# Kernel optimization log

Measured on AMD Instinct MI355X. Metric: run time of the kernel, lower is better.

## Reference

```python
import jax, jax.numpy as jnp
import numpy as np

B, N, E, D, AD = 2, 4096, 4, 64, 32


def setup_inputs() -> dict:
    key = jax.random.key(0)
    ks = jax.random.split(key, 10)
    s = 0.02  # init std matching module _initialization
    return {
        "prop_state": jax.random.normal(ks[0], (B, N, D), jnp.float32),
        "annotation": jax.random.normal(ks[1], (B, N, AD), jnp.float32),
        "A": jax.random.uniform(ks[2], (B, N, N * E), jnp.float32),
        "W_in": jax.random.normal(ks[3], (E, D, D), jnp.float32) * s,
        "b_in": jnp.zeros((E, D), jnp.float32),
        "Wr": jax.random.normal(ks[4], (D, 2 * D), jnp.float32) * s,
        "br": jnp.zeros((D,), jnp.float32),
        "Wz": jax.random.normal(ks[5], (D, 2 * D), jnp.float32) * s,
        "bz": jnp.zeros((D,), jnp.float32),
        "Wh": jax.random.normal(ks[6], (D, 2 * D), jnp.float32) * s,
        "bh": jnp.zeros((D,), jnp.float32),
        "Wo1": jax.random.normal(ks[7], (D, D + AD), jnp.float32) * s,
        "bo1": jnp.zeros((D,), jnp.float32),
        "Wo2": jax.random.normal(ks[8], (1, D), jnp.float32) * s,
        "bo2": jnp.zeros((1,), jnp.float32),
    }


def reference(prop_state, annotation, A, W_in, b_in, Wr, br, Wz, bz, Wh, bh, Wo1, bo1, Wo2, bo2):
    b, n, d = prop_state.shape
    e = W_in.shape[0]
    # per-edge-type input transforms: [B, E, N, D] -> [B, E*N, D] (edge-type major)
    in_states = jnp.einsum('bnd,eod->beno', prop_state, W_in) + b_in[None, :, None, :]
    in_flat = in_states.reshape(b, e * n, d)
    # dense adjacency aggregation: A [B, N, N*E] x in_flat [B, N*E, D]
    a_in = jnp.einsum('bnm,bmd->bnd', A, in_flat)
    # GRU-style gated node update
    a = jnp.concatenate([a_in, prop_state], axis=-1)  # [B, N, 2D]
    r = jax.nn.sigmoid(a @ Wr.T + br)
    z = jax.nn.sigmoid(a @ Wz.T + bz)
    h_hat = jnp.tanh(jnp.concatenate([a_in, r * prop_state], axis=-1) @ Wh.T + bh)
    new_state = (1.0 - z) * prop_state + z * h_hat  # [B, N, D]
    # output head
    join = jnp.concatenate([new_state, annotation], axis=-1)  # [B, N, D+AD]
    h = jnp.tanh(join @ Wo1.T + bo1)
    out = (h @ Wo2.T + bo2).sum(axis=2)  # [B, N]
    return out
```

## Files before the change

kernel.cpp:

```cpp
#include <hip/hip_runtime.h>
#include <hip/hip_bf16.h>
#include <stdint.h>

typedef __bf16 bf16x8 __attribute__((ext_vector_type(8)));
typedef float  f32x16 __attribute__((ext_vector_type(16)));
typedef float  f32x4  __attribute__((ext_vector_type(4)));

static constexpr int Bz = 2, Nn = 4096, Ee = 4, Dd = 64, ADim = 32;
static constexpr int Mm = Nn * Ee;
static constexpr int KSEG = 8;
static constexpr int KLEN = Mm / KSEG;
static constexpr int NT = Bz * Nn / 32;
static constexpr size_t SEGSTRIDE = (size_t)NT * 32 * 64;
static constexpr int PHK = 256;
static constexpr int NPH = KLEN / PHK;

__device__ __forceinline__ bf16x8 cvt8(float4 a, float4 b) {
  bf16x8 r;
  r[0] = (__bf16)a.x; r[1] = (__bf16)a.y; r[2] = (__bf16)a.z; r[3] = (__bf16)a.w;
  r[4] = (__bf16)b.x; r[5] = (__bf16)b.y; r[6] = (__bf16)b.z; r[7] = (__bf16)b.w;
  return r;
}
__device__ __forceinline__ bf16x8 cvt8v(f32x4 a, f32x4 b) {
  bf16x8 r;
  r[0] = (__bf16)a[0]; r[1] = (__bf16)a[1]; r[2] = (__bf16)a[2]; r[3] = (__bf16)a[3];
  r[4] = (__bf16)b[0]; r[5] = (__bf16)b[1]; r[6] = (__bf16)b[2]; r[7] = (__bf16)b[3];
  return r;
}
__device__ __forceinline__ f32x16 zero16() {
  f32x16 z;
#pragma unroll
  for (int i = 0; i < 16; ++i) z[i] = 0.f;
  return z;
}
__device__ __forceinline__ f32x16 mm(bf16x8 a, bf16x8 b, f32x16 c) {
  return __builtin_amdgcn_mfma_f32_32x32x16_bf16(a, b, c, 0, 0, 0);
}
__device__ __forceinline__ float sigm(float x) { return 1.f / (1.f + __expf(-x)); }
__device__ __forceinline__ float tanh_fast(float x) {
  float e = __expf(2.f * x);
  return 1.f - 2.f / (e + 1.f);
}
__device__ __forceinline__ void async_lds16(const void* g, void* l) {
  __builtin_amdgcn_global_load_lds(
      (const __attribute__((address_space(1))) uint32_t*)g,
      (__attribute__((address_space(3))) uint32_t*)l, 16, 0, 0);
}

__global__ __launch_bounds__(256) void k_packbt(
    const float* __restrict__ prop, const float* __restrict__ Win,
    const float* __restrict__ bin, __bf16* __restrict__ Bt,
    const float* __restrict__ Wr, const float* __restrict__ Wz,
    const float* __restrict__ Wh, const float* __restrict__ Wo1,
    __bf16* __restrict__ Wp) {
  const int bid = blockIdx.x;
  const int tid = threadIdx.x;
  const int w = tid >> 6, l = tid & 63;
  const int r31 = l & 31, h = l >> 5;

  if (bid == 512) {
    for (int f = w; f < 60; f += 4) {
      const float* W; int L, fl;
      if (f < 16)      { W = Wr;  L = 128; fl = f; }
      else if (f < 32) { W = Wz;  L = 128; fl = f - 16; }
      else if (f < 48) { W = Wh;  L = 128; fl = f - 32; }
      else             { W = Wo1; L = 96;  fl = f - 48; }
      const int ks = fl >> 1, oh = fl & 1;
      const float* src = W + (size_t)(32 * oh + r31) * L + 16 * ks + 8 * h;
      float4 s0 = *reinterpret_cast<const float4*>(src);
      float4 s1 = *reinterpret_cast<const float4*>(src + 4);
      *reinterpret_cast<bf16x8*>(Wp + ((size_t)f * 64 + l) * 8) = cvt8(s0, s1);
    }
    return;
  }
  const int nchunk = bid & 63;
  const int e = (bid >> 6) & 3, b = bid >> 8;
  const int oh = w & 1, ns = w >> 1;
  const int o_row = oh * 32 + r31;
  const int n_col = nchunk * 64 + ns * 32 + r31;
  const float* wbase = Win + ((size_t)e * 64 + o_row) * 64 + 8 * h;
  const float* pbase = prop + ((size_t)b * Nn + n_col) * 64 + 8 * h;
  f32x16 acc = zero16();
#pragma unroll
  for (int ks = 0; ks < 4; ++ks) {
    float4 w0 = *reinterpret_cast<const float4*>(wbase + 16 * ks);
    float4 w1 = *reinterpret_cast<const float4*>(wbase + 16 * ks + 4);
    float4 p0 = *reinterpret_cast<const float4*>(pbase + 16 * ks);
    float4 p1 = *reinterpret_cast<const float4*>(pbase + 16 * ks + 4);
    acc = mm(cvt8(w0, w1), cvt8(p0, p1), acc);
  }
#pragma unroll
  for (int reg = 0; reg < 16; ++reg) {
    int orow = oh * 32 + (reg & 3) + 8 * (reg >> 2) + 4 * h;
    float v = acc[reg] + bin[e * 64 + orow];
    Bt[((size_t)b * 64 + orow) * Mm + (size_t)e * Nn + n_col] = (__bf16)v;
  }
}

__global__ __launch_bounds__(512, 1) void k_big_gemm(
    const float* __restrict__ A, const __bf16* __restrict__ Bt,
    __bf16* __restrict__ part) {
  __shared__ float  ahalf[2][64][PHK];
  __shared__ __bf16 btl[64][PHK];

  const int bid = blockIdx.x;
  const int kseg = bid & 7;
  const int tg   = bid >> 3;
  const int bb   = tg >> 4;
  const int gg   = tg & 15;
  const int ph0  = tg & (NPH - 1);
  const int tid = threadIdx.x;
  const int w = tid >> 6, l = tid & 63;
  const int r31 = l & 31, h = l >> 5;
  const int tp = w >> 2, q = (w >> 1) & 1, kh = w & 1;

  const size_t kbase = (size_t)kseg * KLEN;
  const float*  Ab  = A  + ((size_t)bb * Nn + gg * 256) * Mm + kbase;
  const __bf16* BtB = Bt + (size_t)bb * 64 * Mm + kbase;

#define ISSUE_A(pi, pr, hf)                                                  \
  { _Pragma("unroll")                                                        \
    for (int j_ = 0; j_ < 8; ++j_) {                                         \
      const int rw_ = 8 * w + j_;                                            \
      const float* src_ = Ab + (size_t)((pi) * 64 + rw_) * Mm +              \
                          (size_t)(pr) * PHK + ((l ^ (rw_ & 7)) << 2);       \
      async_lds16(src_, (void*)&ahalf[hf][rw_][0]);                          \
    } }

  bf16x8 btreg[4];
  const int btrh = l >> 5;
  const int btu  = l & 31;
#define LOAD_BT(pr)                                                          \
  { _Pragma("unroll")                                                        \
    for (int j_ = 0; j_ < 4; ++j_) {                                         \
      const int row_ = 8 * w + 2 * j_ + btrh;                                \
      btreg[j_] = *reinterpret_cast<const bf16x8*>(                          \
          BtB + (size_t)row_ * Mm + (size_t)(pr) * PHK + btu * 8);           \
    } }
#define WRITE_BT                                                             \
  { _Pragma("unroll")                                                        \
    for (int j_ = 0; j_ < 4; ++j_) {                                         \
      const int row_ = 8 * w + 2 * j_ + btrh;                                \
      *reinterpret_cast<bf16x8*>(&btl[row_][(btu ^ (row_ & 7)) * 8]) =       \
          btreg[j_];                                                         \
    } }

  const int swz  = r31 & 7;
  const int arow = tp * 32 + r31;
  const int brow = 32 * q + r31;
  f32x16 acc[4] = {zero16(), zero16(), zero16(), zero16()};

#define COMPUTE(pi, hf)                                                      \
  { _Pragma("unroll")                                                        \
    for (int s_ = 0; s_ < 8; ++s_) {                                         \
      const int ua_ = kh * 32 + 4 * s_ + 2 * h;                              \
      f32x4 fa0 = *reinterpret_cast<const f32x4*>(                           \
          &ahalf[hf][arow][((ua_ ^ swz) << 2)]);                             \
      f32x4 fa1 = *reinterpret_cast<const f32x4*>(                           \
          &ahalf[hf][arow][(((ua_ + 1) ^ swz) << 2)]);                       \
      const int ub_ = kh * 16 + 2 * s_ + h;                                  \
      bf16x8 fb = *reinterpret_cast<const bf16x8*>(                          \
          &btl[brow][((ub_ ^ swz) * 8)]);                                    \
      acc[pi] = mm(cvt8v(fa0, fa1), fb, acc[pi]);                            \
    } }

  LOAD_BT(ph0);
  ISSUE_A(0, ph0, 0);
  ISSUE_A(1, ph0, 1);
  asm volatile("s_waitcnt vmcnt(16)" ::: "memory");
  WRITE_BT;
  asm volatile("s_waitcnt vmcnt(8) lgkmcnt(0)" ::: "memory");
  __builtin_amdgcn_s_barrier();

  for (int pp = 0; pp < NPH; ++pp) {
    const bool lastp = (pp == NPH - 1);
    const int prc = (pp + ph0) & (NPH - 1);
    const int prn = (pp + 1 + ph0) & (NPH - 1);
    COMPUTE(0, 0);
    __builtin_amdgcn_s_barrier();
    ISSUE_A(2, prc, 0);
    asm volatile("s_waitcnt vmcnt(8)" ::: "memory");
    __builtin_amdgcn_s_barrier();
    COMPUTE(1, 1);
    __builtin_amdgcn_s_barrier();
    if (!lastp) LOAD_BT(prn);
    ISSUE_A(3, prc, 1);
    asm volatile("s_waitcnt vmcnt(8)" ::: "memory");
    __builtin_amdgcn_s_barrier();
    COMPUTE(2, 0);
    __builtin_amdgcn_s_barrier();
    if (!lastp) {
      ISSUE_A(0, prn, 0);
      asm volatile("s_waitcnt vmcnt(8)" ::: "memory");
    } else {
      asm volatile("s_waitcnt vmcnt(0)" ::: "memory");
    }
    __builtin_amdgcn_s_barrier();
    COMPUTE(3, 1);
    if (!lastp) {
      __builtin_amdgcn_s_barrier();
      WRITE_BT;
      ISSUE_A(1, prn, 1);
      asm volatile("s_waitcnt vmcnt(8) lgkmcnt(0)" ::: "memory");
      __builtin_amdgcn_s_barrier();
    }
  }
#undef ISSUE_A
#undef LOAD_BT
#undef WRITE_BT
#undef COMPUTE

  float* scratch = &ahalf[0][0][0];
  if (kh == 1) {
#pragma unroll
    for (int i = 0; i < 4; ++i) {
      float* slot = scratch + (size_t)(i * 4 + tp * 2 + q) * 1024 + l * 16;
#pragma unroll
      for (int r = 0; r < 16; r += 4) {
        f32x4 v; v[0] = acc[i][r]; v[1] = acc[i][r + 1];
        v[2] = acc[i][r + 2]; v[3] = acc[i][r + 3];
        *reinterpret_cast<f32x4*>(slot + r) = v;
      }
    }
  }
  __syncthreads();
  if (kh == 0) {
#pragma unroll
    for (int i = 0; i < 4; ++i) {
      const int tile = bb * 128 + gg * 8 + i * 2 + tp;
      __bf16* pb = part + (size_t)kseg * SEGSTRIDE + (size_t)tile * 32 * 64 + 32 * q;
      const float* slot = scratch + (size_t)(i * 4 + tp * 2 + q) * 1024 + l * 16;
#pragma unroll
      for (int reg = 0; reg < 16; ++reg) {
        int row = (reg & 3) + 8 * (reg >> 2) + 4 * h;
        pb[row * 64 + r31] = (__bf16)(acc[i][reg] + slot[reg]);
      }
    }
  }
}

__global__ __launch_bounds__(64) void k_gru(
    const __bf16* __restrict__ part, const float* __restrict__ prop,
    const float* __restrict__ annot, const __bf16* __restrict__ Wp,
    const float* __restrict__ br, const float* __restrict__ bz,
    const float* __restrict__ bh, const float* __restrict__ bo1,
    const float* __restrict__ Wo2, const float* __restrict__ bo2,
    float* __restrict__ out) {
  __shared__ float plds[32][68];
  __shared__ float tlds[32][68];
  const int tile = blockIdx.x;
  const int R0 = tile * 32;
  const int l = threadIdx.x;
  const int r31 = l & 31, h = l >> 5;

  bf16x8 xa[4], xp[4], xan[2];
  {
    const __bf16* pt = part + ((size_t)tile * 32 + r31) * 64 + 8 * h;
    const float* pb = prop + (size_t)(R0 + r31) * 64 + 8 * h;
#pragma unroll
    for (int ks = 0; ks < 4; ++ks) {
      float s[8] = {0.f, 0.f, 0.f, 0.f, 0.f, 0.f, 0.f, 0.f};
#pragma unroll
      for (int seg = 0; seg < KSEG; ++seg) {
        bf16x8 v = *reinterpret_cast<const bf16x8*>(pt + seg * SEGSTRIDE + 16 * ks);
#pragma unroll
        for (int j = 0; j < 8; ++j) s[j] += (float)v[j];
      }
      bf16x8 x;
#pragma unroll
      for (int j = 0; j < 8; ++j) x[j] = (__bf16)s[j];
      xa[ks] = x;
      float4 p0 = *reinterpret_cast<const float4*>(pb + 16 * ks);
      float4 p1 = *reinterpret_cast<const float4*>(pb + 16 * ks + 4);
      xp[ks] = cvt8(p0, p1);
      *reinterpret_cast<float4*>(&plds[r31][16 * ks + 8 * h]) = p0;
      *reinterpret_cast<float4*>(&plds[r31][16 * ks + 8 * h + 4]) = p1;
    }
    const float* anb = annot + (size_t)(R0 + r31) * ADim + 8 * h;
#pragma unroll
    for (int ks = 0; ks < 2; ++ks) {
      float4 a0 = *reinterpret_cast<const float4*>(anb + 16 * ks);
      float4 a1 = *reinterpret_cast<const float4*>(anb + 16 * ks + 4);
      xan[ks] = cvt8(a0, a1);
    }
  }
  __syncthreads();

#define LDWP(base, ks, oh) \
  (*reinterpret_cast<const bf16x8*>(Wp + (((size_t)(base) + (ks) * 2 + (oh)) * 64 + l) * 8))

  f32x16 aR[2] = {zero16(), zero16()}, aZ[2] = {zero16(), zero16()};
#pragma unroll
  for (int ks = 0; ks < 8; ++ks) {
    bf16x8 af = (ks < 4) ? xa[ks] : xp[ks - 4];
#pragma unroll
    for (int oh = 0; oh < 2; ++oh) {
      aR[oh] = mm(af, LDWP(0, ks, oh), aR[oh]);
      aZ[oh] = mm(af, LDWP(16, ks, oh), aZ[oh]);
    }
  }
  const float br_[2] = {br[r31], br[32 + r31]};
  const float bz_[2] = {bz[r31], bz[32 + r31]};
  float propv[2][16], zv[2][16];
#pragma unroll
  for (int oh = 0; oh < 2; ++oh) {
#pragma unroll
    for (int reg = 0; reg < 16; ++reg) {
      int row = (reg & 3) + 8 * (reg >> 2) + 4 * h;
      int o = 32 * oh + r31;
      propv[oh][reg] = plds[row][o];
      float rv = sigm(aR[oh][reg] + br_[oh]);
      zv[oh][reg] = sigm(aZ[oh][reg] + bz_[oh]);
      tlds[row][o] = rv * propv[oh][reg];
    }
  }
  __syncthreads();
  bf16x8 xr[4];
#pragma unroll
  for (int ks = 0; ks < 4; ++ks) {
    float4 t0 = *reinterpret_cast<const float4*>(&tlds[r31][16 * ks + 8 * h]);
    float4 t1 = *reinterpret_cast<const float4*>(&tlds[r31][16 * ks + 8 * h + 4]);
    xr[ks] = cvt8(t0, t1);
  }
  f32x16 aH[2] = {zero16(), zero16()};
#pragma unroll
  for (int ks = 0; ks < 8; ++ks) {
    bf16x8 af = (ks < 4) ? xa[ks] : xr[ks - 4];
#pragma unroll
    for (int oh = 0; oh < 2; ++oh) aH[oh] = mm(af, LDWP(32, ks, oh), aH[oh]);
  }
  __syncthreads();
  const float bh_[2] = {bh[r31], bh[32 + r31]};
#pragma unroll
  for (int oh = 0; oh < 2; ++oh) {
#pragma unroll
    for (int reg = 0; reg < 16; ++reg) {
      int row = (reg & 3) + 8 * (reg >> 2) + 4 * h;
      int o = 32 * oh + r31;
      float hh = tanh_fast(aH[oh][reg] + bh_[oh]);
      float z = zv[oh][reg];
      tlds[row][o] = (1.f - z) * propv[oh][reg] + z * hh;
    }
  }
  __syncthreads();
  bf16x8 xn[4];
#pragma unroll
  for (int ks = 0; ks < 4; ++ks) {
    float4 t0 = *reinterpret_cast<const float4*>(&tlds[r31][16 * ks + 8 * h]);
    float4 t1 = *reinterpret_cast<const float4*>(&tlds[r31][16 * ks + 8 * h + 4]);
    xn[ks] = cvt8(t0, t1);
  }
  f32x16 aO[2] = {zero16(), zero16()};
#pragma unroll
  for (int ks = 0; ks < 6; ++ks) {
    bf16x8 af = (ks < 4) ? xn[ks] : xan[ks - 4];
#pragma unroll
    for (int oh = 0; oh < 2; ++oh) aO[oh] = mm(af, LDWP(48, ks, oh), aO[oh]);
  }
  const float bo1_[2] = {bo1[r31], bo1[32 + r31]};
  const float wo2_[2] = {Wo2[r31], Wo2[32 + r31]};
  const float bo2v = bo2[0];
#pragma unroll
  for (int reg = 0; reg < 16; ++reg) {
    float h0 = tanh_fast(aO[0][reg] + bo1_[0]);
    float h1 = tanh_fast(aO[1][reg] + bo1_[1]);
    float p = h0 * wo2_[0] + h1 * wo2_[1];
#pragma unroll
    for (int mks = 16; mks >= 1; mks >>= 1) p += __shfl_xor(p, mks, 64);
    if (r31 == 0) {
      int row = (reg & 3) + 8 * (reg >> 2) + 4 * h;
      out[R0 + row] = p + bo2v;
    }
  }
#undef LDWP
}

extern "C" void kernel_launch(void* const* d_in, const int* in_sizes, int n_in,
                              void* d_out, int out_size, void* d_ws, size_t ws_size,
                              hipStream_t stream) {
  const float* prop  = (const float*)d_in[0];
  const float* annot = (const float*)d_in[1];
  const float* A     = (const float*)d_in[2];
  const float* Win   = (const float*)d_in[3];
  const float* bin   = (const float*)d_in[4];
  const float* Wr    = (const float*)d_in[5];
  const float* br    = (const float*)d_in[6];
  const float* Wz    = (const float*)d_in[7];
  const float* bz    = (const float*)d_in[8];
  const float* Wh    = (const float*)d_in[9];
  const float* bh    = (const float*)d_in[10];
  const float* Wo1   = (const float*)d_in[11];
  const float* bo1   = (const float*)d_in[12];
  const float* Wo2   = (const float*)d_in[13];
  const float* bo2   = (const float*)d_in[14];
  float* out = (float*)d_out;

  char* ws = (char*)d_ws;
  __bf16* Bt   = (__bf16*)ws;
  __bf16* part = (__bf16*)(ws + (size_t)4 * 1024 * 1024);
  __bf16* Wp   = (__bf16*)(ws + (size_t)16 * 1024 * 1024);

  k_packbt<<<dim3(513), 256, 0, stream>>>(prop, Win, bin, Bt,
                                          Wr, Wz, Wh, Wo1, Wp);
  k_big_gemm<<<dim3(256), 512, 0, stream>>>(A, Bt, part);
  k_gru<<<dim3(NT), 64, 0, stream>>>(part, prop, annot, Wp,
                                     br, bz, bh, bo1, Wo2, bo2, out);
}
```

Measured before the change: 134.0 us.

## Split GRU kernel output columns across two waves and make partials tile-contiguous

```diff
diff --git a/kernel.cpp b/kernel.cpp
--- a/kernel.cpp
+++ b/kernel.cpp
@@ -11,7 +11,6 @@
 static constexpr int KSEG = 8;
 static constexpr int KLEN = Mm / KSEG;
 static constexpr int NT = Bz * Nn / 32;
-static constexpr size_t SEGSTRIDE = (size_t)NT * 32 * 64;
 static constexpr int PHK = 256;
 static constexpr int NPH = KLEN / PHK;
 
@@ -228,7 +227,7 @@
 #pragma unroll
     for (int i = 0; i < 4; ++i) {
       const int tile = bb * 128 + gg * 8 + i * 2 + tp;
-      __bf16* pb = part + (size_t)kseg * SEGSTRIDE + (size_t)tile * 32 * 64 + 32 * q;
+      __bf16* pb = part + ((size_t)tile * KSEG + kseg) * 2048 + 32 * q;
       const float* slot = scratch + (size_t)(i * 4 + tp * 2 + q) * 1024 + l * 16;
 #pragma unroll
       for (int reg = 0; reg < 16; ++reg) {
@@ -239,7 +238,7 @@
   }
 }
 
-__global__ __launch_bounds__(64) void k_gru(
+__global__ __launch_bounds__(128) void k_gru(
     const __bf16* __restrict__ part, const float* __restrict__ prop,
     const float* __restrict__ annot, const __bf16* __restrict__ Wp,
     const float* __restrict__ br, const float* __restrict__ bz,
@@ -248,21 +247,24 @@
     float* __restrict__ out) {
   __shared__ float plds[32][68];
   __shared__ float tlds[32][68];
+  __shared__ float sred[32];
   const int tile = blockIdx.x;
   const int R0 = tile * 32;
-  const int l = threadIdx.x;
+  const int tid = threadIdx.x;
+  const int wv = tid >> 6;
+  const int l = tid & 63;
   const int r31 = l & 31, h = l >> 5;
 
   bf16x8 xa[4], xp[4], xan[2];
   {
-    const __bf16* pt = part + ((size_t)tile * 32 + r31) * 64 + 8 * h;
+    const __bf16* pt = part + (size_t)tile * (KSEG * 2048) + (size_t)r31 * 64 + 8 * h;
     const float* pb = prop + (size_t)(R0 + r31) * 64 + 8 * h;
 #pragma unroll
     for (int ks = 0; ks < 4; ++ks) {
       float s[8] = {0.f, 0.f, 0.f, 0.f, 0.f, 0.f, 0.f, 0.f};
 #pragma unroll
       for (int seg = 0; seg < KSEG; ++seg) {
-        bf16x8 v = *reinterpret_cast<const bf16x8*>(pt + seg * SEGSTRIDE + 16 * ks);
+        bf16x8 v = *reinterpret_cast<const bf16x8*>(pt + seg * 2048 + 16 * ks);
 #pragma unroll
         for (int j = 0; j < 8; ++j) s[j] += (float)v[j];
       }
@@ -273,8 +275,10 @@
       float4 p0 = *reinterpret_cast<const float4*>(pb + 16 * ks);
       float4 p1 = *reinterpret_cast<const float4*>(pb + 16 * ks + 4);
       xp[ks] = cvt8(p0, p1);
-      *reinterpret_cast<float4*>(&plds[r31][16 * ks + 8 * h]) = p0;
-      *reinterpret_cast<float4*>(&plds[r31][16 * ks + 8 * h + 4]) = p1;
+      if (wv == 0) {
+        *reinterpret_cast<float4*>(&plds[r31][16 * ks + 8 * h]) = p0;
+        *reinterpret_cast<float4*>(&plds[r31][16 * ks + 8 * h + 4]) = p1;
+      }
     }
     const float* anb = annot + (size_t)(R0 + r31) * ADim + 8 * h;
 #pragma unroll
@@ -289,30 +293,24 @@
 #define LDWP(base, ks, oh) \
   (*reinterpret_cast<const bf16x8*>(Wp + (((size_t)(base) + (ks) * 2 + (oh)) * 64 + l) * 8))
 
-  f32x16 aR[2] = {zero16(), zero16()}, aZ[2] = {zero16(), zero16()};
+  f32x16 aR = zero16(), aZ = zero16();
 #pragma unroll
   for (int ks = 0; ks < 8; ++ks) {
     bf16x8 af = (ks < 4) ? xa[ks] : xp[ks - 4];
-#pragma unroll
-    for (int oh = 0; oh < 2; ++oh) {
-      aR[oh] = mm(af, LDWP(0, ks, oh), aR[oh]);
-      aZ[oh] = mm(af, LDWP(16, ks, oh), aZ[oh]);
-    }
-  }
-  const float br_[2] = {br[r31], br[32 + r31]};
-  const float bz_[2] = {bz[r31], bz[32 + r31]};
-  float propv[2][16], zv[2][16];
-#pragma unroll
-  for (int oh = 0; oh < 2; ++oh) {
-#pragma unroll
-    for (int reg = 0; reg < 16; ++reg) {
-      int row = (reg & 3) + 8 * (reg >> 2) + 4 * h;
-      int o = 32 * oh + r31;
-      propv[oh][reg] = plds[row][o];
-      float rv = sigm(aR[oh][reg] + br_[oh]);
-      zv[oh][reg] = sigm(aZ[oh][reg] + bz_[oh]);
-      tlds[row][o] = rv * propv[oh][reg];
-    }
+    aR = mm(af, LDWP(0, ks, wv), aR);
+    aZ = mm(af, LDWP(16, ks, wv), aZ);
+  }
+  const float br_ = br[32 * wv + r31];
+  const float bz_ = bz[32 * wv + r31];
+  float propv[16], zv[16];
+  const int oc = 32 * wv + r31;
+#pragma unroll
+  for (int reg = 0; reg < 16; ++reg) {
+    int row = (reg & 3) + 8 * (reg >> 2) + 4 * h;
+    propv[reg] = plds[row][oc];
+    float rv = sigm(aR[reg] + br_);
+    zv[reg] = sigm(aZ[reg] + bz_);
+    tlds[row][oc] = rv * propv[reg];
   }
   __syncthreads();
   bf16x8 xr[4];
@@ -322,25 +320,20 @@
     float4 t1 = *reinterpret_cast<const float4*>(&tlds[r31][16 * ks + 8 * h + 4]);
     xr[ks] = cvt8(t0, t1);
   }
-  f32x16 aH[2] = {zero16(), zero16()};
+  f32x16 aH = zero16();
 #pragma unroll
   for (int ks = 0; ks < 8; ++ks) {
     bf16x8 af = (ks < 4) ? xa[ks] : xr[ks - 4];
-#pragma unroll
-    for (int oh = 0; oh < 2; ++oh) aH[oh] = mm(af, LDWP(32, ks, oh), aH[oh]);
-  }
-  __syncthreads();
-  const float bh_[2] = {bh[r31], bh[32 + r31]};
-#pragma unroll
-  for (int oh = 0; oh < 2; ++oh) {
-#pragma unroll
-    for (int reg = 0; reg < 16; ++reg) {
-      int row = (reg & 3) + 8 * (reg >> 2) + 4 * h;
-      int o = 32 * oh + r31;
-      float hh = tanh_fast(aH[oh][reg] + bh_[oh]);
-      float z = zv[oh][reg];
-      tlds[row][o] = (1.f - z) * propv[oh][reg] + z * hh;
-    }
+    aH = mm(af, LDWP(32, ks, wv), aH);
+  }
+  __syncthreads();
+  const float bh_ = bh[32 * wv + r31];
+#pragma unroll
+  for (int reg = 0; reg < 16; ++reg) {
+    int row = (reg & 3) + 8 * (reg >> 2) + 4 * h;
+    float hh = tanh_fast(aH[reg] + bh_);
+    float z = zv[reg];
+    tlds[row][oc] = (1.f - z) * propv[reg] + z * hh;
   }
   __syncthreads();
   bf16x8 xn[4];
@@ -350,26 +343,33 @@
     float4 t1 = *reinterpret_cast<const float4*>(&tlds[r31][16 * ks + 8 * h + 4]);
     xn[ks] = cvt8(t0, t1);
   }
-  f32x16 aO[2] = {zero16(), zero16()};
+  f32x16 aO = zero16();
 #pragma unroll
   for (int ks = 0; ks < 6; ++ks) {
     bf16x8 af = (ks < 4) ? xn[ks] : xan[ks - 4];
-#pragma unroll
-    for (int oh = 0; oh < 2; ++oh) aO[oh] = mm(af, LDWP(48, ks, oh), aO[oh]);
-  }
-  const float bo1_[2] = {bo1[r31], bo1[32 + r31]};
-  const float wo2_[2] = {Wo2[r31], Wo2[32 + r31]};
+    aO = mm(af, LDWP(48, ks, wv), aO);
+  }
+  const float bo1_ = bo1[32 * wv + r31];
+  const float wo2_ = Wo2[32 * wv + r31];
   const float bo2v = bo2[0];
+  float pred[16];
 #pragma unroll
   for (int reg = 0; reg < 16; ++reg) {
-    float h0 = tanh_fast(aO[0][reg] + bo1_[0]);
-    float h1 = tanh_fast(aO[1][reg] + bo1_[1]);
-    float p = h0 * wo2_[0] + h1 * wo2_[1];
+    float p = tanh_fast(aO[reg] + bo1_) * wo2_;
 #pragma unroll
     for (int mks = 16; mks >= 1; mks >>= 1) p += __shfl_xor(p, mks, 64);
-    if (r31 == 0) {
+    pred[reg] = p;
+  }
+  if (wv == 1 && r31 == 0) {
+#pragma unroll
+    for (int reg = 0; reg < 16; ++reg) sred[reg * 2 + h] = pred[reg];
+  }
+  __syncthreads();
+  if (wv == 0 && r31 == 0) {
+#pragma unroll
+    for (int reg = 0; reg < 16; ++reg) {
       int row = (reg & 3) + 8 * (reg >> 2) + 4 * h;
-      out[R0 + row] = p + bo2v;
+      out[R0 + row] = pred[reg] + sred[reg * 2 + h] + bo2v;
     }
   }
 #undef LDWP
@@ -403,6 +403,6 @@
   k_packbt<<<dim3(513), 256, 0, stream>>>(prop, Win, bin, Bt,
                                           Wr, Wz, Wh, Wo1, Wp);
   k_big_gemm<<<dim3(256), 512, 0, stream>>>(A, Bt, part);
-  k_gru<<<dim3(NT), 64, 0, stream>>>(part, prop, annot, Wp,
-                                     br, bz, bh, bo1, Wo2, bo2, out);
-}
+  k_gru<<<dim3(NT), 128, 0, stream>>>(part, prop, annot, Wp,
+                                      br, bz, bh, bo1, Wo2, bo2, out);
+}
```

New measurement: 127.8 us, median of 2. 4.6% less time.
